# Kernel tuning notes

Hardware: AMD Instinct MI355X
Metric: run time of the kernel (lower is better)

Reference implementation:

```python
import jax, jax.numpy as jnp
import numpy as np

O, I, B = 4096, 4096, 4096  # out_features, in_features, flattened tokens
GROUP = 128
INIT_PEAK = 2.0


def setup_inputs() -> dict:
    key = jax.random.key(0)
    k1, k2, k3, k4 = jax.random.split(key, 4)
    x = jax.random.normal(k1, (B, I), jnp.float32)
    # initial_ternary in {-1,0,1} -> theta init per the torch constructor
    tern = jax.random.randint(k2, (O, I), -1, 2)
    theta_neg = jnp.where(tern == -1, INIT_PEAK, -INIT_PEAK).astype(jnp.float32)
    theta_pos = jnp.where(tern == 1, INIT_PEAK, -INIT_PEAK).astype(jnp.float32)
    # per-group scales expanded to full weight shape (scales.unsqueeze(1).expand.reshape)
    n_groups = O * I // GROUP
    scales = jax.random.uniform(k3, (n_groups,), jnp.float32, 0.01, 0.05)
    scales_exp = jnp.repeat(scales, GROUP).reshape(O, I)
    # reparameterization noise (training path), made explicit for determinism
    eps = jax.random.normal(k4, (B, O), jnp.float32)
    return {"x": x, "theta_neg": theta_neg, "theta_pos": theta_pos,
            "scales_exp": scales_exp, "eps": eps}


def reference(x, theta_neg, theta_pos, scales_exp, eps):
    # stable 3-way softmax over logits [theta_neg, 0, theta_pos], done without
    # materializing the stacked [O, I, 3] tensor
    m = jnp.maximum(jnp.maximum(theta_neg, theta_pos), 0.0)
    e_neg = jnp.exp(theta_neg - m)
    e_zero = jnp.exp(-m)
    e_pos = jnp.exp(theta_pos - m)
    Z = e_neg + e_zero + e_pos
    p_neg = e_neg / Z
    p_pos = e_pos / Z
    diff = p_pos - p_neg
    w_mean = diff * scales_exp                                   # [O, I]
    w_var = (p_pos + p_neg - diff * diff) * (scales_exp * scales_exp)  # [O, I]
    mu = x @ w_mean.T                                            # [B, O]
    sigma_sq = (x * x) @ w_var.T                                 # [B, O]
    sigma = jnp.sqrt(jnp.maximum(sigma_sq, 1e-8))
    return mu + sigma * eps
```

## Files before the change

kernel.cpp:

```cpp
#include <hip/hip_runtime.h>

#define I_DIM 4096
#define O_DIM 4096
#define B_DIM 4096

typedef __bf16 bf16;
typedef __attribute__((ext_vector_type(8))) __bf16 bf16x8;
typedef __attribute__((ext_vector_type(4))) float f32x4;
typedef __attribute__((ext_vector_type(8))) unsigned short ushort8;

__device__ inline unsigned short f2bf_bits(float f) {
    unsigned u = __builtin_bit_cast(unsigned, f);
    unsigned r = 0x7fffu + ((u >> 16) & 1u);
    return (unsigned short)((u + r) >> 16);
}

__device__ inline void lr_wmv(float tn, float tp, float s,
                              unsigned short& wm, unsigned short& wv) {
    float m = fmaxf(fmaxf(tn, tp), 0.0f);
    float en = __expf(tn - m);
    float ez = __expf(-m);
    float ep = __expf(tp - m);
    float inv = __builtin_amdgcn_rcpf(en + ez + ep);
    float pn = en * inv, pp = ep * inv;
    float d = pp - pn;
    wm = f2bf_bits(d * s);
    wv = f2bf_bits((pp + pn - d * d) * (s * s));
}

__global__ void prep_all(const float4* __restrict__ x,
                         ushort8* __restrict__ xb8, ushort8* __restrict__ x2b8,
                         const float4* __restrict__ tn, const float4* __restrict__ tp,
                         const float4* __restrict__ sc,
                         ushort4* __restrict__ wm, ushort4* __restrict__ wv,
                         int nbx) {
    const int bid = blockIdx.x;
    if (bid < nbx) {
        size_t i = (size_t)bid * blockDim.x + threadIdx.x;
        float4 a = x[2 * i];
        float4 b = x[2 * i + 1];
        ushort8 o1, o2;
        o1[0] = f2bf_bits(a.x); o1[1] = f2bf_bits(a.y);
        o1[2] = f2bf_bits(a.z); o1[3] = f2bf_bits(a.w);
        o1[4] = f2bf_bits(b.x); o1[5] = f2bf_bits(b.y);
        o1[6] = f2bf_bits(b.z); o1[7] = f2bf_bits(b.w);
        o2[0] = f2bf_bits(a.x * a.x); o2[1] = f2bf_bits(a.y * a.y);
        o2[2] = f2bf_bits(a.z * a.z); o2[3] = f2bf_bits(a.w * a.w);
        o2[4] = f2bf_bits(b.x * b.x); o2[5] = f2bf_bits(b.y * b.y);
        o2[6] = f2bf_bits(b.z * b.z); o2[7] = f2bf_bits(b.w * b.w);
        xb8[i] = o1;
        x2b8[i] = o2;
    } else {
        size_t i = (size_t)(bid - nbx) * blockDim.x + threadIdx.x;
        float4 a = tn[i];
        float4 b = tp[i];
        float4 s = sc[i];
        ushort4 om, ov;
        lr_wmv(a.x, b.x, s.x, om.x, ov.x);
        lr_wmv(a.y, b.y, s.y, om.y, ov.y);
        lr_wmv(a.z, b.z, s.z, om.z, ov.z);
        lr_wmv(a.w, b.w, s.w, om.w, ov.w);
        wm[i] = om;
        wv[i] = ov;
    }
}

#define BM 128
#define BN 128
#define BK 64

__device__ inline void gl_lds16(const bf16* g, bf16* l) {
    __builtin_amdgcn_global_load_lds(
        (const __attribute__((address_space(1))) unsigned int*)g,
        (__attribute__((address_space(3))) unsigned int*)l,
        16, 0, 0);
}

__global__ __launch_bounds__(256, 2)
void fused_dual_gemm(const bf16* __restrict__ Xb, const bf16* __restrict__ X2b,
                     const bf16* __restrict__ Wm, const bf16* __restrict__ Wv,
                     const float* __restrict__ eps, float* __restrict__ out) {
    __shared__ bf16 sX[BM * BK];
    __shared__ bf16 sX2[BM * BK];
    __shared__ bf16 sWm[BN * BK];
    __shared__ bf16 sWv[BN * BK];

    const int tid  = threadIdx.x;
    const int lane = tid & 63;
    const int wave = tid >> 6;

    const int bm = blockIdx.y * BM;
    const int bn = blockIdx.x * BN;

    const int rowoff = lane >> 3;
    const int cgoff  = ((lane & 7) ^ rowoff) << 3;

    const bf16* gX[4]; const bf16* gX2[4]; const bf16* gWm[4]; const bf16* gWv[4];
    int ldsoff[4];
#pragma unroll
    for (int j = 0; j < 4; ++j) {
        const int c = wave + 4 * j;
        const size_t ra = (size_t)(bm + c * 8 + rowoff) * I_DIM + cgoff;
        const size_t rb = (size_t)(bn + c * 8 + rowoff) * I_DIM + cgoff;
        gX[j]  = Xb  + ra;
        gX2[j] = X2b + ra;
        gWm[j] = Wm  + rb;
        gWv[j] = Wv  + rb;
        ldsoff[j] = c << 9;
    }

    const int fr  = lane & 15;
    const int cg0 = lane >> 4;
    const int sw0 = (cg0 ^ (fr & 7)) << 3;
    const int m0 = (wave >> 1) << 6;
    const int n0 = (wave & 1) << 6;

    f32x4 accM[4][4];
    f32x4 accV[4][4];
    const f32x4 z = {0.0f, 0.0f, 0.0f, 0.0f};
#pragma unroll
    for (int mi = 0; mi < 4; ++mi)
#pragma unroll
        for (int ni = 0; ni < 4; ++ni) { accM[mi][ni] = z; accV[mi][ni] = z; }

    for (int k0 = 0; k0 < I_DIM; k0 += BK) {
        __syncthreads();
#pragma unroll
        for (int j = 0; j < 4; ++j) {
            gl_lds16(gX[j]  + k0, sX  + ldsoff[j]);
            gl_lds16(gX2[j] + k0, sX2 + ldsoff[j]);
            gl_lds16(gWm[j] + k0, sWm + ldsoff[j]);
            gl_lds16(gWv[j] + k0, sWv + ldsoff[j]);
        }
        __syncthreads();

#pragma unroll
        for (int kh = 0; kh < 2; ++kh) {
            const int sw = sw0 ^ (kh << 5);
            bf16x8 ax[4], ax2[4];
#pragma unroll
            for (int mi = 0; mi < 4; ++mi) {
                const int row = m0 + mi * 16 + fr;
                ax[mi]  = *(const bf16x8*)&sX [row * BK + sw];
                ax2[mi] = *(const bf16x8*)&sX2[row * BK + sw];
            }
#pragma unroll
            for (int ni = 0; ni < 4; ++ni) {
                const int rowb = n0 + ni * 16 + fr;
                bf16x8 bm_ = *(const bf16x8*)&sWm[rowb * BK + sw];
                bf16x8 bv_ = *(const bf16x8*)&sWv[rowb * BK + sw];
#pragma unroll
                for (int mi = 0; mi < 4; ++mi) {
                    accM[mi][ni] = __builtin_amdgcn_mfma_f32_16x16x32_bf16(
                        ax[mi], bm_, accM[mi][ni], 0, 0, 0);
                    accV[mi][ni] = __builtin_amdgcn_mfma_f32_16x16x32_bf16(
                        ax2[mi], bv_, accV[mi][ni], 0, 0, 0);
                }
            }
        }
    }

    const int oc  = lane & 15;
    const int orb = (lane >> 4) << 2;
#pragma unroll
    for (int mi = 0; mi < 4; ++mi) {
#pragma unroll
        for (int ni = 0; ni < 4; ++ni) {
            const int gn = bn + n0 + ni * 16 + oc;
            const int gm = bm + m0 + mi * 16 + orb;
#pragma unroll
            for (int r = 0; r < 4; ++r) {
                const size_t off = (size_t)(gm + r) * O_DIM + gn;
                const float mu = accM[mi][ni][r];
                const float vv = accV[mi][ni][r];
                out[off] = fmaf(sqrtf(fmaxf(vv, 1e-8f)), eps[off], mu);
            }
        }
    }
}

extern "C" void kernel_launch(void* const* d_in, const int* in_sizes, int n_in,
                              void* d_out, int out_size, void* d_ws, size_t ws_size,
                              hipStream_t stream) {
    const float* x   = (const float*)d_in[0];
    const float* tn  = (const float*)d_in[1];
    const float* tp  = (const float*)d_in[2];
    const float* sc  = (const float*)d_in[3];
    const float* eps = (const float*)d_in[4];
    float* out = (float*)d_out;

    const size_t NE = (size_t)O_DIM * I_DIM;
    unsigned short* xb  = (unsigned short*)d_ws;
    unsigned short* x2b = xb + NE;
    unsigned short* wm  = x2b + NE;
    unsigned short* wv  = wm + NE;

    const int nbx = (int)(NE / 8 / 256);
    const int nbw = (int)(NE / 4 / 256);
    prep_all<<<nbx + nbw, 256, 0, stream>>>(
        (const float4*)x, (ushort8*)xb, (ushort8*)x2b,
        (const float4*)tn, (const float4*)tp, (const float4*)sc,
        (ushort4*)wm, (ushort4*)wv, nbx);

    dim3 grid(O_DIM / BN, B_DIM / BM);
    fused_dual_gemm<<<grid, 256, 0, stream>>>(
        (const bf16*)xb, (const bf16*)x2b, (const bf16*)wm, (const bf16*)wv, eps, out);
}
```

Baseline: 610.9 us.

## Split mean and variance GEMMs across waves with narrower N tile

Result: slower. 659.8 us (+8.0%).

```diff
diff --git a/kernel.cpp b/kernel.cpp
--- a/kernel.cpp
+++ b/kernel.cpp
@@ -66,7 +66,7 @@
 }
 
 #define BM 128
-#define BN 128
+#define BN 64
 #define BK 64
 
 __device__ inline void gl_lds16(const bf16* g, bf16* l) {
@@ -76,14 +76,15 @@
         16, 0, 0);
 }
 
-__global__ __launch_bounds__(256, 2)
+__global__ __launch_bounds__(256, 3)
 void fused_dual_gemm(const bf16* __restrict__ Xb, const bf16* __restrict__ X2b,
                      const bf16* __restrict__ Wm, const bf16* __restrict__ Wv,
                      const float* __restrict__ eps, float* __restrict__ out) {
-    __shared__ bf16 sX[BM * BK];
-    __shared__ bf16 sX2[BM * BK];
-    __shared__ bf16 sWm[BN * BK];
-    __shared__ bf16 sWv[BN * BK];
+    __shared__ char smem[49152];
+    bf16* sX  = (bf16*)(smem);
+    bf16* sX2 = (bf16*)(smem + 16384);
+    bf16* sWm = (bf16*)(smem + 32768);
+    bf16* sWv = (bf16*)(smem + 40960);
 
     const int tid  = threadIdx.x;
     const int lane = tid & 63;
@@ -95,85 +96,100 @@
     const int rowoff = lane >> 3;
     const int cgoff  = ((lane & 7) ^ rowoff) << 3;
 
-    const bf16* gX[4]; const bf16* gX2[4]; const bf16* gWm[4]; const bf16* gWv[4];
-    int ldsoff[4];
+    const bf16* gX[4]; const bf16* gX2[4]; int loffX[4];
+    const bf16* gWm[2]; const bf16* gWv[2]; int loffW[2];
 #pragma unroll
     for (int j = 0; j < 4; ++j) {
         const int c = wave + 4 * j;
         const size_t ra = (size_t)(bm + c * 8 + rowoff) * I_DIM + cgoff;
-        const size_t rb = (size_t)(bn + c * 8 + rowoff) * I_DIM + cgoff;
         gX[j]  = Xb  + ra;
         gX2[j] = X2b + ra;
-        gWm[j] = Wm  + rb;
-        gWv[j] = Wv  + rb;
-        ldsoff[j] = c << 9;
-    }
+        loffX[j] = c << 9;
+    }
+#pragma unroll
+    for (int j = 0; j < 2; ++j) {
+        const int c = wave + 4 * j;
+        const size_t rb = (size_t)(bn + c * 8 + rowoff) * I_DIM + cgoff;
+        gWm[j] = Wm + rb;
+        gWv[j] = Wv + rb;
+        loffW[j] = c << 9;
+    }
+
+    const bf16* myA = (wave >= 2) ? sX2 : sX;
+    const bf16* myB = (wave >= 2) ? sWv : sWm;
+    const int m0 = (wave & 1) << 6;
 
     const int fr  = lane & 15;
-    const int cg0 = lane >> 4;
-    const int sw0 = (cg0 ^ (fr & 7)) << 3;
-    const int m0 = (wave >> 1) << 6;
-    const int n0 = (wave & 1) << 6;
-
-    f32x4 accM[4][4];
-    f32x4 accV[4][4];
+    const int sw0 = (((lane >> 4) ^ (fr & 7)) << 3);
+
+    f32x4 acc[4][4];
     const f32x4 z = {0.0f, 0.0f, 0.0f, 0.0f};
 #pragma unroll
     for (int mi = 0; mi < 4; ++mi)
 #pragma unroll
-        for (int ni = 0; ni < 4; ++ni) { accM[mi][ni] = z; accV[mi][ni] = z; }
+        for (int ni = 0; ni < 4; ++ni) acc[mi][ni] = z;
 
     for (int k0 = 0; k0 < I_DIM; k0 += BK) {
         __syncthreads();
 #pragma unroll
         for (int j = 0; j < 4; ++j) {
-            gl_lds16(gX[j]  + k0, sX  + ldsoff[j]);
-            gl_lds16(gX2[j] + k0, sX2 + ldsoff[j]);
-            gl_lds16(gWm[j] + k0, sWm + ldsoff[j]);
-            gl_lds16(gWv[j] + k0, sWv + ldsoff[j]);
+            gl_lds16(gX[j]  + k0, sX  + loffX[j]);
+            gl_lds16(gX2[j] + k0, sX2 + loffX[j]);
+        }
+#pragma unroll
+        for (int j = 0; j < 2; ++j) {
+            gl_lds16(gWm[j] + k0, sWm + loffW[j]);
+            gl_lds16(gWv[j] + k0, sWv + loffW[j]);
         }
         __syncthreads();
 
 #pragma unroll
         for (int kh = 0; kh < 2; ++kh) {
             const int sw = sw0 ^ (kh << 5);
-            bf16x8 ax[4], ax2[4];
-#pragma unroll
-            for (int mi = 0; mi < 4; ++mi) {
-                const int row = m0 + mi * 16 + fr;
-                ax[mi]  = *(const bf16x8*)&sX [row * BK + sw];
-                ax2[mi] = *(const bf16x8*)&sX2[row * BK + sw];
+            bf16x8 a[4];
+#pragma unroll
+            for (int mi = 0; mi < 4; ++mi)
+                a[mi] = *(const bf16x8*)&myA[(m0 + mi * 16 + fr) * BK + sw];
+#pragma unroll
+            for (int ni = 0; ni < 4; ++ni) {
+                bf16x8 b = *(const bf16x8*)&myB[(ni * 16 + fr) * BK + sw];
+#pragma unroll
+                for (int mi = 0; mi < 4; ++mi)
+                    acc[mi][ni] = __builtin_amdgcn_mfma_f32_16x16x32_bf16(
+                        a[mi], b, acc[mi][ni], 0, 0, 0);
             }
+        }
+    }
+
+    __syncthreads();
+    float* xfer = (float*)smem;
+    if (wave >= 2) {
+        float* dst = xfer + ((wave - 2) << 12);
+#pragma unroll
+        for (int mi = 0; mi < 4; ++mi)
+#pragma unroll
+            for (int ni = 0; ni < 4; ++ni)
+#pragma unroll
+                for (int r = 0; r < 4; ++r)
+                    dst[mi * 1024 + ni * 256 + r * 64 + lane] = acc[mi][ni][r];
+    }
+    __syncthreads();
+    if (wave < 2) {
+        const float* src = xfer + (wave << 12);
+        const int oc  = lane & 15;
+        const int orb = (lane >> 4) << 2;
+#pragma unroll
+        for (int mi = 0; mi < 4; ++mi) {
 #pragma unroll
             for (int ni = 0; ni < 4; ++ni) {
-                const int rowb = n0 + ni * 16 + fr;
-                bf16x8 bm_ = *(const bf16x8*)&sWm[rowb * BK + sw];
-                bf16x8 bv_ = *(const bf16x8*)&sWv[rowb * BK + sw];
-#pragma unroll
-                for (int mi = 0; mi < 4; ++mi) {
-                    accM[mi][ni] = __builtin_amdgcn_mfma_f32_16x16x32_bf16(
-                        ax[mi], bm_, accM[mi][ni], 0, 0, 0);
-                    accV[mi][ni] = __builtin_amdgcn_mfma_f32_16x16x32_bf16(
-                        ax2[mi], bv_, accV[mi][ni], 0, 0, 0);
+                const int gn = bn + ni * 16 + oc;
+                const int gm = bm + m0 + mi * 16 + orb;
+#pragma unroll
+                for (int r = 0; r < 4; ++r) {
+                    const float vv = src[mi * 1024 + ni * 256 + r * 64 + lane];
+                    const size_t off = (size_t)(gm + r) * O_DIM + gn;
+                    out[off] = fmaf(sqrtf(fmaxf(vv, 1e-8f)), eps[off], acc[mi][ni][r]);
                 }
-            }
-        }
-    }
-
-    const int oc  = lane & 15;
-    const int orb = (lane >> 4) << 2;
-#pragma unroll
-    for (int mi = 0; mi < 4; ++mi) {
-#pragma unroll
-        for (int ni = 0; ni < 4; ++ni) {
-            const int gn = bn + n0 + ni * 16 + oc;
-            const int gm = bm + m0 + mi * 16 + orb;
-#pragma unroll
-            for (int r = 0; r < 4; ++r) {
-                const size_t off = (size_t)(gm + r) * O_DIM + gn;
-                const float mu = accM[mi][ni][r];
-                const float vv = accV[mi][ni][r];
-                out[off] = fmaf(sqrtf(fmaxf(vv, 1e-8f)), eps[off], mu);
             }
         }
     }
```

## Switch to fp16 and compute x squared in-register instead of storing x2

Applied to the files above, without the earlier changes.

New measurement: 551.2 us. 1.11x faster.

```diff
diff --git a/kernel.cpp b/kernel.cpp
--- a/kernel.cpp
+++ b/kernel.cpp
@@ -4,19 +4,13 @@
 #define O_DIM 4096
 #define B_DIM 4096
 
-typedef __bf16 bf16;
-typedef __attribute__((ext_vector_type(8))) __bf16 bf16x8;
+typedef _Float16 f16;
+typedef __attribute__((ext_vector_type(8))) _Float16 f16x8;
 typedef __attribute__((ext_vector_type(4))) float f32x4;
-typedef __attribute__((ext_vector_type(8))) unsigned short ushort8;
 
-__device__ inline unsigned short f2bf_bits(float f) {
-    unsigned u = __builtin_bit_cast(unsigned, f);
-    unsigned r = 0x7fffu + ((u >> 16) & 1u);
-    return (unsigned short)((u + r) >> 16);
-}
+struct f16pair { f16 m, v; };
 
-__device__ inline void lr_wmv(float tn, float tp, float s,
-                              unsigned short& wm, unsigned short& wv) {
+__device__ inline f16pair lr_wmv(float tn, float tp, float s) {
     float m = fmaxf(fmaxf(tn, tp), 0.0f);
     float en = __expf(tn - m);
     float ez = __expf(-m);
@@ -24,44 +18,43 @@
     float inv = __builtin_amdgcn_rcpf(en + ez + ep);
     float pn = en * inv, pp = ep * inv;
     float d = pp - pn;
-    wm = f2bf_bits(d * s);
-    wv = f2bf_bits((pp + pn - d * d) * (s * s));
+    f16pair r;
+    r.m = (f16)(d * s);
+    r.v = (f16)((pp + pn - d * d) * (s * s));
+    return r;
 }
 
-__global__ void prep_all(const float4* __restrict__ x,
-                         ushort8* __restrict__ xb8, ushort8* __restrict__ x2b8,
-                         const float4* __restrict__ tn, const float4* __restrict__ tp,
-                         const float4* __restrict__ sc,
-                         ushort4* __restrict__ wm, ushort4* __restrict__ wv,
+__global__ void prep_all(const float4* __restrict__ x, f16x8* __restrict__ xb8,
+                         const float4* __restrict__ tn4, const float4* __restrict__ tp4,
+                         const float4* __restrict__ sc4,
+                         f16x8* __restrict__ wm8, f16x8* __restrict__ wv8,
                          int nbx) {
     const int bid = blockIdx.x;
     if (bid < nbx) {
         size_t i = (size_t)bid * blockDim.x + threadIdx.x;
         float4 a = x[2 * i];
         float4 b = x[2 * i + 1];
-        ushort8 o1, o2;
-        o1[0] = f2bf_bits(a.x); o1[1] = f2bf_bits(a.y);
-        o1[2] = f2bf_bits(a.z); o1[3] = f2bf_bits(a.w);
-        o1[4] = f2bf_bits(b.x); o1[5] = f2bf_bits(b.y);
-        o1[6] = f2bf_bits(b.z); o1[7] = f2bf_bits(b.w);
-        o2[0] = f2bf_bits(a.x * a.x); o2[1] = f2bf_bits(a.y * a.y);
-        o2[2] = f2bf_bits(a.z * a.z); o2[3] = f2bf_bits(a.w * a.w);
-        o2[4] = f2bf_bits(b.x * b.x); o2[5] = f2bf_bits(b.y * b.y);
-        o2[6] = f2bf_bits(b.z * b.z); o2[7] = f2bf_bits(b.w * b.w);
-        xb8[i] = o1;
-        x2b8[i] = o2;
+        f16x8 o;
+        o[0] = (f16)a.x; o[1] = (f16)a.y; o[2] = (f16)a.z; o[3] = (f16)a.w;
+        o[4] = (f16)b.x; o[5] = (f16)b.y; o[6] = (f16)b.z; o[7] = (f16)b.w;
+        xb8[i] = o;
     } else {
         size_t i = (size_t)(bid - nbx) * blockDim.x + threadIdx.x;
-        float4 a = tn[i];
-        float4 b = tp[i];
-        float4 s = sc[i];
-        ushort4 om, ov;
-        lr_wmv(a.x, b.x, s.x, om.x, ov.x);
-        lr_wmv(a.y, b.y, s.y, om.y, ov.y);
-        lr_wmv(a.z, b.z, s.z, om.z, ov.z);
-        lr_wmv(a.w, b.w, s.w, om.w, ov.w);
-        wm[i] = om;
-        wv[i] = ov;
+        float4 a0 = tn4[2 * i], a1 = tn4[2 * i + 1];
+        float4 b0 = tp4[2 * i], b1 = tp4[2 * i + 1];
+        float4 s0 = sc4[2 * i], s1 = sc4[2 * i + 1];
+        f16x8 om, ov;
+        f16pair p;
+        p = lr_wmv(a0.x, b0.x, s0.x); om[0] = p.m; ov[0] = p.v;
+        p = lr_wmv(a0.y, b0.y, s0.y); om[1] = p.m; ov[1] = p.v;
+        p = lr_wmv(a0.z, b0.z, s0.z); om[2] = p.m; ov[2] = p.v;
+        p = lr_wmv(a0.w, b0.w, s0.w); om[3] = p.m; ov[3] = p.v;
+        p = lr_wmv(a1.x, b1.x, s1.x); om[4] = p.m; ov[4] = p.v;
+        p = lr_wmv(a1.y, b1.y, s1.y); om[5] = p.m; ov[5] = p.v;
+        p = lr_wmv(a1.z, b1.z, s1.z); om[6] = p.m; ov[6] = p.v;
+        p = lr_wmv(a1.w, b1.w, s1.w); om[7] = p.m; ov[7] = p.v;
+        wm8[i] = om;
+        wv8[i] = ov;
     }
 }
 
@@ -69,7 +62,7 @@
 #define BN 128
 #define BK 64
 
-__device__ inline void gl_lds16(const bf16* g, bf16* l) {
+__device__ inline void gl_lds16(const f16* g, f16* l) {
     __builtin_amdgcn_global_load_lds(
         (const __attribute__((address_space(1))) unsigned int*)g,
         (__attribute__((address_space(3))) unsigned int*)l,
@@ -77,13 +70,11 @@
 }
 
 __global__ __launch_bounds__(256, 2)
-void fused_dual_gemm(const bf16* __restrict__ Xb, const bf16* __restrict__ X2b,
-                     const bf16* __restrict__ Wm, const bf16* __restrict__ Wv,
+void fused_dual_gemm(const f16* __restrict__ Xb,
+                     const f16* __restrict__ Wm, const f16* __restrict__ Wv,
                      const float* __restrict__ eps, float* __restrict__ out) {
-    __shared__ bf16 sX[BM * BK];
-    __shared__ bf16 sX2[BM * BK];
-    __shared__ bf16 sWm[BN * BK];
-    __shared__ bf16 sWv[BN * BK];
+    __shared__ f16 smem[24576];
+    f16* sX  = smem;
 
     const int tid  = threadIdx.x;
     const int lane = tid & 63;
@@ -95,23 +86,21 @@
     const int rowoff = lane >> 3;
     const int cgoff  = ((lane & 7) ^ rowoff) << 3;
 
-    const bf16* gX[4]; const bf16* gX2[4]; const bf16* gWm[4]; const bf16* gWv[4];
-    int ldsoff[4];
+    const f16* g[12];
+    int loff[12];
 #pragma unroll
-    for (int j = 0; j < 4; ++j) {
-        const int c = wave + 4 * j;
-        const size_t ra = (size_t)(bm + c * 8 + rowoff) * I_DIM + cgoff;
-        const size_t rb = (size_t)(bn + c * 8 + rowoff) * I_DIM + cgoff;
-        gX[j]  = Xb  + ra;
-        gX2[j] = X2b + ra;
-        gWm[j] = Wm  + rb;
-        gWv[j] = Wv  + rb;
-        ldsoff[j] = c << 9;
+    for (int j = 0; j < 12; ++j) {
+        const int cj  = wave + 4 * j;
+        const int arr = cj >> 4;
+        const int lc  = cj & 15;
+        const int tb  = (arr == 0) ? bm : bn;
+        const f16* base = (arr == 0) ? Xb : ((arr == 1) ? Wm : Wv);
+        g[j] = base + (size_t)(tb + lc * 8 + rowoff) * I_DIM + cgoff;
+        loff[j] = cj << 9;
     }
 
     const int fr  = lane & 15;
-    const int cg0 = lane >> 4;
-    const int sw0 = (cg0 ^ (fr & 7)) << 3;
+    const int sw0 = (((lane >> 4) ^ (fr & 7)) << 3);
     const int m0 = (wave >> 1) << 6;
     const int n0 = (wave & 1) << 6;
 
@@ -123,38 +112,36 @@
 #pragma unroll
         for (int ni = 0; ni < 4; ++ni) { accM[mi][ni] = z; accV[mi][ni] = z; }
 
+    const f16* sWm = smem + 8192;
+    const f16* sWv = smem + 16384;
+
     for (int k0 = 0; k0 < I_DIM; k0 += BK) {
         __syncthreads();
 #pragma unroll
-        for (int j = 0; j < 4; ++j) {
-            gl_lds16(gX[j]  + k0, sX  + ldsoff[j]);
-            gl_lds16(gX2[j] + k0, sX2 + ldsoff[j]);
-            gl_lds16(gWm[j] + k0, sWm + ldsoff[j]);
-            gl_lds16(gWv[j] + k0, sWv + ldsoff[j]);
-        }
+        for (int j = 0; j < 12; ++j)
+            gl_lds16(g[j] + k0, smem + loff[j]);
         __syncthreads();
 
 #pragma unroll
         for (int kh = 0; kh < 2; ++kh) {
             const int sw = sw0 ^ (kh << 5);
-            bf16x8 ax[4], ax2[4];
+            f16x8 a[4], a2[4];
 #pragma unroll
             for (int mi = 0; mi < 4; ++mi) {
-                const int row = m0 + mi * 16 + fr;
-                ax[mi]  = *(const bf16x8*)&sX [row * BK + sw];
-                ax2[mi] = *(const bf16x8*)&sX2[row * BK + sw];
+                a[mi]  = *(const f16x8*)&sX[(m0 + mi * 16 + fr) * BK + sw];
+                a2[mi] = a[mi] * a[mi];
             }
 #pragma unroll
             for (int ni = 0; ni < 4; ++ni) {
-                const int rowb = n0 + ni * 16 + fr;
-                bf16x8 bm_ = *(const bf16x8*)&sWm[rowb * BK + sw];
-                bf16x8 bv_ = *(const bf16x8*)&sWv[rowb * BK + sw];
+                const int rowb = (n0 + ni * 16 + fr) * BK + sw;
+                f16x8 bm_ = *(const f16x8*)&sWm[rowb];
+                f16x8 bv_ = *(const f16x8*)&sWv[rowb];
 #pragma unroll
                 for (int mi = 0; mi < 4; ++mi) {
-                    accM[mi][ni] = __builtin_amdgcn_mfma_f32_16x16x32_bf16(
-                        ax[mi], bm_, accM[mi][ni], 0, 0, 0);
-                    accV[mi][ni] = __builtin_amdgcn_mfma_f32_16x16x32_bf16(
-                        ax2[mi], bv_, accV[mi][ni], 0, 0, 0);
+                    accM[mi][ni] = __builtin_amdgcn_mfma_f32_16x16x32_f16(
+                        a[mi], bm_, accM[mi][ni], 0, 0, 0);
+                    accV[mi][ni] = __builtin_amdgcn_mfma_f32_16x16x32_f16(
+                        a2[mi], bv_, accV[mi][ni], 0, 0, 0);
                 }
             }
         }
@@ -190,19 +177,18 @@
     float* out = (float*)d_out;
 
     const size_t NE = (size_t)O_DIM * I_DIM;
-    unsigned short* xb  = (unsigned short*)d_ws;
-    unsigned short* x2b = xb + NE;
-    unsigned short* wm  = x2b + NE;
-    unsigned short* wv  = wm + NE;
+    f16* xb = (f16*)d_ws;
+    f16* wm = xb + NE;
+    f16* wv = wm + NE;
 
     const int nbx = (int)(NE / 8 / 256);
-    const int nbw = (int)(NE / 4 / 256);
+    const int nbw = (int)(NE / 8 / 256);
     prep_all<<<nbx + nbw, 256, 0, stream>>>(
-        (const float4*)x, (ushort8*)xb, (ushort8*)x2b,
+        (const float4*)x, (f16x8*)xb,
         (const float4*)tn, (const float4*)tp, (const float4*)sc,
-        (ushort4*)wm, (ushort4*)wv, nbx);
+        (f16x8*)wm, (f16x8*)wv, nbx);
 
     dim3 grid(O_DIM / BN, B_DIM / BM);
     fused_dual_gemm<<<grid, 256, 0, stream>>>(
-        (const bf16*)xb, (const bf16*)x2b, (const bf16*)wm, (const bf16*)wv, eps, out);
+        (const f16*)xb, (const f16*)wm, (const f16*)wv, eps, out);
 }
```
